# Performance work log

Hardware: AMD Instinct MI355X
Metric: run time of the kernel (lower is better)

Reference implementation:

```python
import jax, jax.numpy as jnp
import numpy as np

T, B, C = 2048, 4, 512
H, K, P = 16, 31, 15  # num_heads, kernel_size, padding_l
R = C // H


def setup_inputs() -> dict:
    key = jax.random.key(0)
    ks = jax.random.split(key, 6)
    x = jax.random.normal(ks[0], (T, B, C), dtype=jnp.float32)
    s = 0.02
    W1 = jax.random.normal(ks[1], (C, C), dtype=jnp.float32) * s   # linear1 weight
    b1 = jnp.zeros((C,), dtype=jnp.float32)
    Wl = jax.random.normal(ks[2], (H * K, C), dtype=jnp.float32) * s  # weight_linear (no bias)
    W2 = jax.random.normal(ks[3], (C, C), dtype=jnp.float32) * s   # linear2 weight
    b2 = jnp.zeros((C,), dtype=jnp.float32)
    return {"x": x, "W1": W1, "b1": b1, "Wl": Wl, "W2": W2, "b2": b2}


def _dynamic_conv(h, Wl):
    # h: (T, B, C). Generate per-position per-head filters, softmax over K,
    # then banded weighted sum over a local window of K timesteps.
    w = jnp.einsum('tbc,kc->tbk', h, Wl).reshape(T, B, H, K)
    w = jax.nn.softmax(w, axis=-1)                      # weight_softmax=True
    # pad left P, right K-1-P ("same" window: position t sees h[t-P : t-P+K])
    hp = jnp.pad(h, ((P, K - 1 - P), (0, 0), (0, 0)))   # (T+K-1, B, C)
    idx = jnp.arange(T)[:, None] + jnp.arange(K)[None, :]  # (T, K)
    hw = hp[idx].reshape(T, K, B, H, R)                 # unfolded windows
    return jnp.einsum('tkbhr,tbhk->tbhr', hw, w).reshape(T, B, C)


def reference(x, W1, b1, Wl, W2, b2):
    h = jnp.einsum('tbc,dc->tbd', x, W1) + b1           # linear1 (glu=False -> no act)
    out = _dynamic_conv(h, Wl)                          # conv_bias=False
    out = jnp.einsum('tbc,dc->tbd', out, W2) + b2       # linear2
    return out
```

## Files before the change

### kernel.cpp

```cpp
#include <hip/hip_runtime.h>
#include <hip/hip_bf16.h>

#define TT 2048
#define BB 4
#define CC 512
#define HH 16
#define KK 31
#define PP 15
#define MM (TT*BB)
#define NPAD 512

typedef __bf16 bf16x8 __attribute__((ext_vector_type(8)));
typedef float f32x4 __attribute__((ext_vector_type(4)));
typedef unsigned short ushort8 __attribute__((ext_vector_type(8)));
typedef unsigned short ushort4v __attribute__((ext_vector_type(4)));

__device__ __forceinline__ float bf2f(unsigned short u) {
    return __uint_as_float(((unsigned int)u) << 16);
}
__device__ __forceinline__ unsigned short f2bf(float f) {
    unsigned int x = __float_as_uint(f);
    x += 0x7fffu + ((x >> 16) & 1u);
    return (unsigned short)(x >> 16);
}

__global__ __launch_bounds__(256) void cast_all(const float* __restrict__ x,
                                                const float* __restrict__ W1,
                                                const float* __restrict__ Wl,
                                                const float* __restrict__ W2,
                                                unsigned short* __restrict__ xb,
                                                unsigned short* __restrict__ W1b,
                                                unsigned short* __restrict__ Wlb,
                                                unsigned short* __restrict__ W2b) {
    const int b = blockIdx.x;
    if (b < 4096) {
        const int i = b * 1024 + threadIdx.x * 4;
        const float4 v = *(const float4*)&x[i];
        ushort4v o = { f2bf(v.x), f2bf(v.y), f2bf(v.z), f2bf(v.w) };
        *(ushort4v*)&xb[i] = o;
        return;
    }
    const int bb = b - 4096;
    const int i = (bb & 255) * 1024 + threadIdx.x * 4;
    const float* src;
    unsigned short* dst;
    int n_src = 262144;
    if (bb < 256)      { src = W1; dst = W1b; }
    else if (bb < 512) { src = Wl; dst = Wlb; n_src = HH * KK * CC; }
    else               { src = W2; dst = W2b; }
    ushort4v o = {0, 0, 0, 0};
    if (i < n_src) {
        const float4 v = *(const float4*)&src[i];
        o[0] = f2bf(v.x); o[1] = f2bf(v.y); o[2] = f2bf(v.z); o[3] = f2bf(v.w);
    }
    *(ushort4v*)&dst[i] = o;
}

#define GBM 128
#define GBN 64
#define GBK 64
#define KC  512
#define NT  8

#define STAGE(kt, buf)                                                                             \
    do {                                                                                           \
        const int k0_ = (kt) * GBK;                                                                \
        _Pragma("unroll")                                                                          \
        for (int j = 0; j < 2; ++j)                                                                \
            __builtin_amdgcn_global_load_lds(                                                      \
                (const __attribute__((address_space(1))) void*)(gA[j] + k0_),                      \
                (__attribute__((address_space(3))) void*)(&As[buf][0] + (j * 512 + wv * 64) * 8),  \
                16, 0, 0);                                                                         \
        __builtin_amdgcn_global_load_lds(                                                          \
            (const __attribute__((address_space(1))) void*)(gB0 + k0_),                            \
            (__attribute__((address_space(3))) void*)(&Bs[buf][0] + wv * 64 * 8),                  \
            16, 0, 0);                                                                             \
    } while (0)

template<bool OUT_BF16>
__global__ __launch_bounds__(512, 4) void gemm_nt_mfma(const unsigned short* __restrict__ A,
                                                       const unsigned short* __restrict__ B,
                                                       const float* __restrict__ bias,
                                                       void* __restrict__ Cout,
                                                       int N, int nn) {
    __shared__ short As[3][GBM * GBK];
    __shared__ short Bs[3][GBN * GBK];

    const int tid = threadIdx.x;
    const int l   = tid & 63;
    const int wv  = tid >> 6;
    const int wr  = wv >> 1;
    const int wc  = wv & 1;

    const int s  = (blockIdx.x & 7) * (gridDim.x >> 3) + (blockIdx.x >> 3);
    const int bm = (s / nn) * GBM;
    const int bn = (s % nn) * GBN;

    const unsigned short* gA[2];
    #pragma unroll
    for (int j = 0; j < 2; ++j) {
        const int slot = j * 512 + tid;
        const int r  = slot >> 3;
        const int sl = (slot & 7) ^ (r & 7);
        gA[j] = A + (size_t)(bm + r) * KC + sl * 8;
    }
    const int rB  = tid >> 3;
    const int slB = (tid & 7) ^ (rB & 7);
    const unsigned short* gB0 = B + (size_t)(bn + rB) * KC + slB * 8;

    f32x4 acc[2][2] = {};

    const int lr = l & 15;
    const int ls = l >> 4;
    int offA[2][2], offB[2][2];
    #pragma unroll
    for (int mi = 0; mi < 2; ++mi) {
        const int r = wr * 32 + mi * 16 + lr;
        #pragma unroll
        for (int ks = 0; ks < 2; ++ks)
            offA[mi][ks] = r * 64 + (((ks * 4 + ls) ^ (r & 7)) * 8);
    }
    #pragma unroll
    for (int ni = 0; ni < 2; ++ni) {
        const int r = wc * 32 + ni * 16 + lr;
        #pragma unroll
        for (int ks = 0; ks < 2; ++ks)
            offB[ni][ks] = r * 64 + (((ks * 4 + ls) ^ (r & 7)) * 8);
    }

    STAGE(0, 0);
    STAGE(1, 1);

    #pragma unroll
    for (int kt = 0; kt < NT; ++kt) {
        if (kt < NT - 1) asm volatile("s_waitcnt vmcnt(3)" ::: "memory");
        else             asm volatile("s_waitcnt vmcnt(0)" ::: "memory");
        __builtin_amdgcn_s_barrier();
        if (kt + 2 < NT) STAGE(kt + 2, (kt + 2) % 3);

        const int cb = kt % 3;
        bf16x8 af[2][2], bfv[2][2];
        #pragma unroll
        for (int mi = 0; mi < 2; ++mi)
            #pragma unroll
            for (int ks = 0; ks < 2; ++ks)
                af[mi][ks] = *(const bf16x8*)&As[cb][offA[mi][ks]];
        #pragma unroll
        for (int ni = 0; ni < 2; ++ni)
            #pragma unroll
            for (int ks = 0; ks < 2; ++ks)
                bfv[ni][ks] = *(const bf16x8*)&Bs[cb][offB[ni][ks]];

        #pragma unroll
        for (int mi = 0; mi < 2; ++mi)
            #pragma unroll
            for (int ni = 0; ni < 2; ++ni)
                #pragma unroll
                for (int ks = 0; ks < 2; ++ks)
                    acc[mi][ni] = __builtin_amdgcn_mfma_f32_16x16x32_bf16(af[mi][ks], bfv[ni][ks], acc[mi][ni], 0, 0, 0);
    }

    #pragma unroll
    for (int mi = 0; mi < 2; ++mi) {
        const int row0 = bm + wr * 32 + mi * 16 + ls * 4;
        #pragma unroll
        for (int ni = 0; ni < 2; ++ni) {
            const int col = bn + wc * 32 + ni * 16 + lr;
            const float bv = bias ? bias[col] : 0.0f;
            #pragma unroll
            for (int j = 0; j < 4; ++j) {
                const float v = acc[mi][ni][j] + bv;
                if (OUT_BF16)
                    ((unsigned short*)Cout)[(size_t)(row0 + j) * N + col] = f2bf(v);
                else
                    ((float*)Cout)[(size_t)(row0 + j) * N + col] = v;
            }
        }
    }
}

__global__ __launch_bounds__(64) void dynconv_fused(const unsigned short* __restrict__ hb,
                                                    const unsigned short* __restrict__ lgb,
                                                    unsigned short* __restrict__ cvb) {
    __shared__ float w_s[64][33];

    const int bid = blockIdx.x;
    const int u   = (bid & 7) * 256 + (bid >> 3);
    const int tg  = u >> 2;
    const int b   = u & 3;
    const int t0  = tg * 4;
    const int tid = threadIdx.x;

    {
        const int dt = tid >> 4, hd = tid & 15;
        const unsigned short* lp = lgb + (size_t)((t0 + dt) * BB + b) * NPAD + hd * KK;
        float e[KK];
        float mx = -1e30f;
        #pragma unroll
        for (int k = 0; k < KK; ++k) { e[k] = bf2f(lp[k]); mx = fmaxf(mx, e[k]); }
        float sm = 0.f;
        #pragma unroll
        for (int k = 0; k < KK; ++k) { e[k] = __expf(e[k] - mx); sm += e[k]; }
        const float inv = 1.f / sm;
        #pragma unroll
        for (int k = 0; k < KK; ++k) w_s[tid][k] = e[k] * inv;
    }
    __syncthreads();

    const int c0 = tid * 8;
    const int hd = tid >> 2;
    float acc[4][8] = {};
    #pragma unroll
    for (int j = 0; j < 34; ++j) {
        const int tt = t0 - PP + j;
        if ((unsigned)tt >= TT) continue;
        const ushort8 hv = *(const ushort8*)&hb[(size_t)((tt * BB + b) * CC) + c0];
        float hf[8];
        #pragma unroll
        for (int cc = 0; cc < 8; ++cc) hf[cc] = bf2f(hv[cc]);
        #pragma unroll
        for (int dt = 0; dt < 4; ++dt) {
            const int k = j - dt;
            if (k < 0 || k >= KK) continue;
            const float wk = w_s[dt * 16 + hd][k];
            #pragma unroll
            for (int cc = 0; cc < 8; ++cc) acc[dt][cc] = fmaf(hf[cc], wk, acc[dt][cc]);
        }
    }
    #pragma unroll
    for (int dt = 0; dt < 4; ++dt) {
        ushort8 o;
        #pragma unroll
        for (int cc = 0; cc < 8; ++cc) o[cc] = f2bf(acc[dt][cc]);
        *(ushort8*)&cvb[(size_t)(((t0 + dt) * BB + b) * CC) + c0] = o;
    }
}

extern "C" void kernel_launch(void* const* d_in, const int* in_sizes, int n_in,
                              void* d_out, int out_size, void* d_ws, size_t ws_size,
                              hipStream_t stream) {
    const float* x  = (const float*)d_in[0];
    const float* W1 = (const float*)d_in[1];
    const float* b1 = (const float*)d_in[2];
    const float* Wl = (const float*)d_in[3];
    const float* W2 = (const float*)d_in[4];
    const float* b2 = (const float*)d_in[5];
    float* out = (float*)d_out;

    unsigned short* xb  = (unsigned short*)d_ws;
    unsigned short* hb  = xb  + (size_t)MM * CC;
    unsigned short* cvb = hb  + (size_t)MM * CC;
    unsigned short* W1b = cvb + (size_t)MM * CC;
    unsigned short* Wlb = W1b + (size_t)CC * CC;
    unsigned short* W2b = Wlb + (size_t)NPAD * CC;
    unsigned short* lgb = W2b + (size_t)CC * CC;

    cast_all<<<4096 + 768, 256, 0, stream>>>(x, W1, Wl, W2, xb, W1b, Wlb, W2b);

    const int nblk = (MM / GBM) * (CC / GBN);

    gemm_nt_mfma<true><<<nblk, 512, 0, stream>>>(xb, W1b, b1, hb, CC, CC / GBN);
    gemm_nt_mfma<true><<<nblk, 512, 0, stream>>>(hb, Wlb, nullptr, lgb, NPAD, NPAD / GBN);
    dynconv_fused<<<TT * BB / 4, 64, 0, stream>>>(hb, lgb, cvb);
    gemm_nt_mfma<false><<<nblk, 512, 0, stream>>>(cvb, W2b, b2, out, CC, CC / GBN);
}
```

Measured before the change: 50.36 us.

## Fuse fp32-to-bf16 casts into GEMM tile loads, drop separate cast kernel

Removes the standalone cast kernel and instead has the GEMM load fp32 operands (x for the first GEMM, all weight matrices) through registers, converting to bf16 and writing into LDS in a software-pipelined fashion. This eliminates one launch and the extra round trip of writing and rereading bf16 copies of x and the weights. In exchange, the weights are re-converted by every block, fp32 loads double the global traffic for those operands, and the async global-to-LDS path is replaced by register staging for B and for A in the first GEMM.

After: 51.96 us. 1.03x slower.

```diff
diff --git a/kernel.cpp b/kernel.cpp
--- a/kernel.cpp
+++ b/kernel.cpp
@@ -13,7 +13,6 @@
 typedef __bf16 bf16x8 __attribute__((ext_vector_type(8)));
 typedef float f32x4 __attribute__((ext_vector_type(4)));
 typedef unsigned short ushort8 __attribute__((ext_vector_type(8)));
-typedef unsigned short ushort4v __attribute__((ext_vector_type(4)));
 
 __device__ __forceinline__ float bf2f(unsigned short u) {
     return __uint_as_float(((unsigned int)u) << 16);
@@ -22,38 +21,6 @@
     unsigned int x = __float_as_uint(f);
     x += 0x7fffu + ((x >> 16) & 1u);
     return (unsigned short)(x >> 16);
-}
-
-__global__ __launch_bounds__(256) void cast_all(const float* __restrict__ x,
-                                                const float* __restrict__ W1,
-                                                const float* __restrict__ Wl,
-                                                const float* __restrict__ W2,
-                                                unsigned short* __restrict__ xb,
-                                                unsigned short* __restrict__ W1b,
-                                                unsigned short* __restrict__ Wlb,
-                                                unsigned short* __restrict__ W2b) {
-    const int b = blockIdx.x;
-    if (b < 4096) {
-        const int i = b * 1024 + threadIdx.x * 4;
-        const float4 v = *(const float4*)&x[i];
-        ushort4v o = { f2bf(v.x), f2bf(v.y), f2bf(v.z), f2bf(v.w) };
-        *(ushort4v*)&xb[i] = o;
-        return;
-    }
-    const int bb = b - 4096;
-    const int i = (bb & 255) * 1024 + threadIdx.x * 4;
-    const float* src;
-    unsigned short* dst;
-    int n_src = 262144;
-    if (bb < 256)      { src = W1; dst = W1b; }
-    else if (bb < 512) { src = Wl; dst = Wlb; n_src = HH * KK * CC; }
-    else               { src = W2; dst = W2b; }
-    ushort4v o = {0, 0, 0, 0};
-    if (i < n_src) {
-        const float4 v = *(const float4*)&src[i];
-        o[0] = f2bf(v.x); o[1] = f2bf(v.y); o[2] = f2bf(v.z); o[3] = f2bf(v.w);
-    }
-    *(ushort4v*)&dst[i] = o;
 }
 
 #define GBM 128
@@ -62,24 +29,48 @@
 #define KC  512
 #define NT  8
 
-#define STAGE(kt, buf)                                                                             \
-    do {                                                                                           \
-        const int k0_ = (kt) * GBK;                                                                \
-        _Pragma("unroll")                                                                          \
-        for (int j = 0; j < 2; ++j)                                                                \
-            __builtin_amdgcn_global_load_lds(                                                      \
-                (const __attribute__((address_space(1))) void*)(gA[j] + k0_),                      \
-                (__attribute__((address_space(3))) void*)(&As[buf][0] + (j * 512 + wv * 64) * 8),  \
-                16, 0, 0);                                                                         \
-        __builtin_amdgcn_global_load_lds(                                                          \
-            (const __attribute__((address_space(1))) void*)(gB0 + k0_),                            \
-            (__attribute__((address_space(3))) void*)(&Bs[buf][0] + wv * 64 * 8),                  \
-            16, 0, 0);                                                                             \
-    } while (0)
-
-template<bool OUT_BF16>
-__global__ __launch_bounds__(512, 4) void gemm_nt_mfma(const unsigned short* __restrict__ A,
-                                                       const unsigned short* __restrict__ B,
+#define PACK8(lo, hi, dst)                                                      \
+    do { ushort8 o_;                                                            \
+         o_[0] = f2bf((lo).x); o_[1] = f2bf((lo).y);                            \
+         o_[2] = f2bf((lo).z); o_[3] = f2bf((lo).w);                            \
+         o_[4] = f2bf((hi).x); o_[5] = f2bf((hi).y);                            \
+         o_[6] = f2bf((hi).z); o_[7] = f2bf((hi).w);                            \
+         *(ushort8*)(dst) = o_; } while (0)
+
+#define LOADB(kt, d)                                                            \
+    do { float4 z_ = make_float4(0.f, 0.f, 0.f, 0.f);                           \
+         bLo[d] = z_; bHi[d] = z_;                                              \
+         if (bok) { bLo[d] = *(const float4*)(gBf + (kt) * GBK);                \
+                    bHi[d] = *(const float4*)(gBf + (kt) * GBK + 4); } } while (0)
+
+#define WRITEB(kt, d) PACK8(bLo[d], bHi[d], &Bs[(kt) % 3][rB * 64 + psB * 8])
+
+#define LOADA_F(kt, d)                                                          \
+    do { _Pragma("unroll")                                                      \
+         for (int j_ = 0; j_ < 2; ++j_) {                                       \
+             aLo[d][j_] = *(const float4*)(gAf[j_] + (kt) * GBK);               \
+             aHi[d][j_] = *(const float4*)(gAf[j_] + (kt) * GBK + 4);           \
+         } } while (0)
+
+#define WRITEA_F(kt, d)                                                         \
+    do { _Pragma("unroll")                                                      \
+         for (int j_ = 0; j_ < 2; ++j_)                                         \
+             PACK8(aLo[d][j_], aHi[d][j_],                                      \
+                   &As[(kt) % 3][rA[j_] * 64 + psA[j_] * 8]); } while (0)
+
+#define STAGEA_G(kt, buf)                                                       \
+    do { const int k0_ = (kt) * GBK;                                            \
+         _Pragma("unroll")                                                      \
+         for (int j_ = 0; j_ < 2; ++j_)                                         \
+             __builtin_amdgcn_global_load_lds(                                  \
+                 (const __attribute__((address_space(1))) void*)(gAg[j_] + k0_),\
+                 (__attribute__((address_space(3))) void*)(&As[buf][0] + (j_ * 512 + wv * 64) * 8), \
+                 16, 0, 0); } while (0)
+
+template<int AF32, int OUT_BF16>
+__global__ __launch_bounds__(512, 4) void gemm_nt_mfma(const void* __restrict__ Aptr,
+                                                       const float* __restrict__ Bf,
+                                                       int nvB,
                                                        const float* __restrict__ bias,
                                                        void* __restrict__ Cout,
                                                        int N, int nn) {
@@ -96,17 +87,26 @@
     const int bm = (s / nn) * GBM;
     const int bn = (s % nn) * GBN;
 
-    const unsigned short* gA[2];
+    const int rB  = tid >> 3;
+    const int pB  = tid & 7;
+    const int psB = pB ^ (rB & 7);
+    const float* gBf = Bf + (size_t)(bn + rB) * KC + pB * 8;
+    const bool bok = (bn + rB) < nvB;
+    float4 bLo[2], bHi[2];
+
+    int rA[2], psA[2];
+    const float* gAf[2];
+    const unsigned short* gAg[2];
     #pragma unroll
     for (int j = 0; j < 2; ++j) {
         const int slot = j * 512 + tid;
-        const int r  = slot >> 3;
-        const int sl = (slot & 7) ^ (r & 7);
-        gA[j] = A + (size_t)(bm + r) * KC + sl * 8;
-    }
-    const int rB  = tid >> 3;
-    const int slB = (tid & 7) ^ (rB & 7);
-    const unsigned short* gB0 = B + (size_t)(bn + rB) * KC + slB * 8;
+        const int r = slot >> 3;
+        const int p = slot & 7;
+        rA[j] = r; psA[j] = p ^ (r & 7);
+        gAf[j] = (const float*)Aptr + (size_t)(bm + r) * KC + p * 8;
+        gAg[j] = (const unsigned short*)Aptr + (size_t)(bm + r) * KC + (p ^ (r & 7)) * 8;
+    }
+    float4 aLo[2][2], aHi[2][2];
 
     f32x4 acc[2][2] = {};
 
@@ -128,15 +128,28 @@
             offB[ni][ks] = r * 64 + (((ks * 4 + ls) ^ (r & 7)) * 8);
     }
 
-    STAGE(0, 0);
-    STAGE(1, 1);
+    LOADB(0, 0);
+    if (AF32) LOADA_F(0, 0); else STAGEA_G(0, 0);
+    LOADB(1, 1);
+    if (AF32) LOADA_F(1, 1); else STAGEA_G(1, 1);
+    WRITEB(0, 0);
+    if (AF32) WRITEA_F(0, 0);
 
     #pragma unroll
     for (int kt = 0; kt < NT; ++kt) {
-        if (kt < NT - 1) asm volatile("s_waitcnt vmcnt(3)" ::: "memory");
-        else             asm volatile("s_waitcnt vmcnt(0)" ::: "memory");
+        if (kt + 1 < NT) {
+            WRITEB(kt + 1, (kt + 1) & 1);
+            if (AF32) WRITEA_F(kt + 1, (kt + 1) & 1);
+        }
+        if (kt + 2 < NT) {
+            LOADB(kt + 2, (kt + 2) & 1);
+            if (AF32) LOADA_F(kt + 2, (kt + 2) & 1);
+        }
+        asm volatile("s_waitcnt lgkmcnt(0)" ::: "memory");
+        if (kt == NT - 1) asm volatile("s_waitcnt vmcnt(0)" ::: "memory");
         __builtin_amdgcn_s_barrier();
-        if (kt + 2 < NT) STAGE(kt + 2, (kt + 2) % 3);
+        asm volatile("" ::: "memory");
+        if (!AF32 && kt + 2 < NT) STAGEA_G(kt + 2, (kt + 2) % 3);
 
         const int cb = kt % 3;
         bf16x8 af[2][2], bfv[2][2];
@@ -247,20 +260,14 @@
     const float* b2 = (const float*)d_in[5];
     float* out = (float*)d_out;
 
-    unsigned short* xb  = (unsigned short*)d_ws;
-    unsigned short* hb  = xb  + (size_t)MM * CC;
+    unsigned short* hb  = (unsigned short*)d_ws;
     unsigned short* cvb = hb  + (size_t)MM * CC;
-    unsigned short* W1b = cvb + (size_t)MM * CC;
-    unsigned short* Wlb = W1b + (size_t)CC * CC;
-    unsigned short* W2b = Wlb + (size_t)NPAD * CC;
-    unsigned short* lgb = W2b + (size_t)CC * CC;
-
-    cast_all<<<4096 + 768, 256, 0, stream>>>(x, W1, Wl, W2, xb, W1b, Wlb, W2b);
+    unsigned short* lgb = cvb + (size_t)MM * CC;
 
     const int nblk = (MM / GBM) * (CC / GBN);
 
-    gemm_nt_mfma<true><<<nblk, 512, 0, stream>>>(xb, W1b, b1, hb, CC, CC / GBN);
-    gemm_nt_mfma<true><<<nblk, 512, 0, stream>>>(hb, Wlb, nullptr, lgb, NPAD, NPAD / GBN);
+    gemm_nt_mfma<1, 1><<<nblk, 512, 0, stream>>>(x, W1, 512, b1, hb, CC, CC / GBN);
+    gemm_nt_mfma<0, 1><<<nblk, 512, 0, stream>>>(hb, Wl, HH * KK, nullptr, lgb, NPAD, NPAD / GBN);
     dynconv_fused<<<TT * BB / 4, 64, 0, stream>>>(hb, lgb, cvb);
-    gemm_nt_mfma<false><<<nblk, 512, 0, stream>>>(cvb, W2b, b2, out, CC, CC / GBN);
-}
+    gemm_nt_mfma<0, 0><<<nblk, 512, 0, stream>>>(cvb, W2, 512, b2, out, CC, CC / GBN);
+}
```
